# Optimization experiments

Measured on AMD Instinct MI355X. Metric: run time of the kernel, lower is better.

Reference implementation:

```python
import jax, jax.numpy as jnp
import numpy as np

EPS = 1e-6

def elu1(x):
    return jax.nn.elu(x) + 1.0

def causal_linear_attention(q, k, v, chunk=128):
    # q,k,v: [b,h,s,d]; standard (elu+1) linear attention with causal cumulative
    # normalization, computed chunk-wise with a lax.scan carrying the kv state.
    b, h, s, d = q.shape
    sq, sk = elu1(q), elu1(k)
    nc = s // chunk
    rs = lambda x: x.reshape(b, h, nc, chunk, d).transpose(2, 0, 1, 3, 4)  # [nc,b,h,L,d]
    sqc, skc, vc = rs(sq), rs(sk), rs(v)
    mask = jnp.tril(jnp.ones((chunk, chunk), dtype=q.dtype))

    def step(carry, xs):
        S, z = carry  # S: [b,h,d,d] running sum of k^T v; z: [b,h,d] running sum of k
        qc, kc, vcc = xs
        scores = jnp.einsum('bhid,bhjd->bhij', qc, kc) * mask
        num = jnp.einsum('bhij,bhje->bhie', scores, vcc) + jnp.einsum('bhid,bhde->bhie', qc, S)
        den = scores.sum(-1) + jnp.einsum('bhid,bhd->bhi', qc, z)
        out = num / jnp.clip(den, EPS)[..., None]
        S = S + jnp.einsum('bhjd,bhje->bhde', kc, vcc)
        z = z + kc.sum(2)
        return (S, z), out

    S0 = jnp.zeros((b, h, d, d), q.dtype)
    z0 = jnp.zeros((b, h, d), q.dtype)
    _, outs = jax.lax.scan(step, (S0, z0), (sqc, skc, vc))
    return outs.transpose(1, 2, 0, 3, 4).reshape(b, h, s, d)

def setup_inputs() -> dict:
    B, S, H, NH, NM = 2, 4096, 2048, 16, 4
    HD = H // NH
    key = jax.random.key(0)
    ks = jax.random.split(key, 12)
    p = lambda k, shp: (jax.random.normal(k, shp, dtype=jnp.float32) * 0.02)
    return {
        'hidden_states': jax.random.normal(ks[0], (B, S, H), dtype=jnp.float32),
        'w_q': p(ks[1], (H, H)),
        'w_k': p(ks[2], (H, H)),
        'w_v': p(ks[3], (H, H)),
        'w_o': p(ks[4], (H, H)),
        'eg_w1': p(ks[5], (H // 4, H)),
        'eg_b1': jnp.zeros((H // 4,), jnp.float32),
        'eg_w2': p(ks[6], (1, H // 4)),
        'eg_b2': jnp.zeros((1,), jnp.float32),
        'memory_gate': jnp.zeros((NH,), jnp.float32),
        'fine_memories': jax.random.uniform(ks[7], (NM, NH, HD, HD), dtype=jnp.float32) * 0.1,
        'fine_memory_norms': jax.random.uniform(ks[8], (NM, NH, HD), dtype=jnp.float32) + 0.1,
    }

def reference(hidden_states, w_q, w_k, w_v, w_o, eg_w1, eg_b1, eg_w2, eg_b2,
              memory_gate, fine_memories, fine_memory_norms):
    B, S, H = hidden_states.shape
    NH = memory_gate.shape[0]
    HD = H // NH
    split = lambda x: x.reshape(B, S, NH, HD).transpose(0, 2, 1, 3)  # [b,h,s,d]
    q = split(hidden_states @ w_q.T)
    k = split(hidden_states @ w_k.T)
    v = split(hidden_states @ w_v.T)
    sq = elu1(q)

    # coarse memory = sum of fine banks
    M = fine_memories.sum(0)            # [h,d,d]
    z = fine_memory_norms.sum(0)        # [h,d]
    a_c = jnp.einsum('bhsd,hde->bhse', sq, M)
    n_c = jnp.clip(jnp.einsum('bhsd,hd->bhs', sq, z), EPS)[..., None]
    out_coarse = jnp.where(z.sum() < EPS, 0.0, a_c / n_c)

    # fine-grained retrieval over banks, softmax-weighted by relevance
    a_f = jnp.einsum('bhsd,mhde->mbhse', sq, fine_memories)
    n_f = jnp.einsum('bhsd,mhd->mbhs', sq, fine_memory_norms)
    bank_dead = (fine_memory_norms.sum((1, 2)) < EPS)[:, None, None, None, None]
    outs = jnp.where(bank_dead, 0.0, a_f / jnp.clip(n_f, EPS)[..., None])
    rel = n_f.mean(-1)  # [m,b,h]
    w = jax.nn.softmax(rel, axis=0)[..., None, None]  # [m,b,h,1,1]
    out_fine = (outs * w).sum(0)

    # learned expansion gate from coarse representation
    coarse_repr = out_coarse.transpose(0, 2, 1, 3).reshape(B, S, H)
    gprob = jax.nn.sigmoid(jax.nn.relu(coarse_repr @ eg_w1.T + eg_b1) @ eg_w2.T + eg_b2)  # [b,s,1]
    exp_prob = gprob.transpose(0, 2, 1)[..., None]  # [b,1,s,1]

    memory_output = exp_prob * out_fine + (1.0 - exp_prob) * out_coarse
    local_output = causal_linear_attention(q, k, v)
    gate = jax.nn.sigmoid(memory_gate).reshape(1, NH, 1, 1)
    output = gate * memory_output + (1.0 - gate) * local_output
    output = output.transpose(0, 2, 1, 3).reshape(B, S, H)
    return output @ w_o.T
```

## Files before the change

kernel.cpp:

```cpp
#include <hip/hip_runtime.h>

typedef unsigned short ush;
typedef short s16x8 __attribute__((ext_vector_type(8)));
typedef float f32x4 __attribute__((ext_vector_type(4)));

#define Bv 2
#define Sv 4096
#define Hv 2048
#define NHv 16
#define HDv 128
#define NMv 4
#define Tv (Bv*Sv)
#define CHv 128
#define NCv (Sv/CHv)
#define EPSf 1e-6f
#define NTHc ((size_t)Tv*Hv)

__device__ __forceinline__ float b2f(ush u){ return __uint_as_float(((unsigned)u)<<16); }
__device__ __forceinline__ ush f2b(float f){
  unsigned x = __float_as_uint(f);
  return (ush)((x + 0x7fffu + ((x>>16)&1u)) >> 16);
}
__device__ __forceinline__ float lo16(unsigned u){ return b2f((ush)(u & 0xffffu)); }
__device__ __forceinline__ float hi16(unsigned u){ return b2f((ush)(u >> 16)); }
__device__ __forceinline__ unsigned pack2(float a, float b){ return (unsigned)f2b(a) | ((unsigned)f2b(b) << 16); }
__device__ __forceinline__ float elu1f(float x){ return x > 0.f ? x + 1.f : __expf(x); }
__device__ __forceinline__ float sigm(float x){ return 1.f/(1.f + __expf(-x)); }

__device__ __forceinline__ void gload_lds16(const ush* g, ush* l) {
  __builtin_amdgcn_global_load_lds((const __attribute__((address_space(1))) unsigned int*)g,
                                   (__attribute__((address_space(3))) unsigned int*)l, 16, 0, 0);
}

__global__ void probe_kernel(float* out, float val){ out[0] = val; }

__global__ __launch_bounds__(256)
void cvt_kernel(const float* __restrict__ in, ush* __restrict__ out, int n8)
{
  int i = blockIdx.x * 256 + threadIdx.x;
  if (i >= n8) return;
  const float4* p = (const float4*)in + (size_t)i*2;
  float4 x = p[0], y = p[1];
  ushort4 a; a.x=f2b(x.x); a.y=f2b(x.y); a.z=f2b(x.z); a.w=f2b(x.w);
  ushort4 b; b.x=f2b(y.x); b.y=f2b(y.y); b.z=f2b(y.z); b.w=f2b(y.w);
  *(ushort4*)(out + (size_t)i*8)     = a;
  *(ushort4*)(out + (size_t)i*8 + 4) = b;
}

__global__ __launch_bounds__(256)
void fmt_kernel(const float* __restrict__ fm, ush* __restrict__ fmt)
{
  int mh = blockIdx.x;
  const float* src = fm + (size_t)mh*HDv*HDv;
  ush* dst = fmt + (size_t)mh*HDv*HDv;
  __shared__ ush T[HDv][HDv+4];
  #pragma unroll 4
  for (int l = 0; l < 64; ++l) {
    int idx = threadIdx.x + l*256;
    int d = idx >> 7, e = idx & 127;
    T[d][e] = f2b(src[idx]);
  }
  __syncthreads();
  #pragma unroll 4
  for (int l = 0; l < 64; ++l) {
    int idx = threadIdx.x + l*256;
    int e = idx >> 7, d = idx & 127;
    dst[idx] = T[d][e];
  }
}

__global__ __launch_bounds__(256)
void tp_kernel(const ush* __restrict__ src, ush* __restrict__ dst)
{
  int blk = blockIdx.x;
  int st = blk & 31, bh = blk >> 5;
  int h = bh & 15, b = bh >> 4;
  size_t t0 = (size_t)b*Sv + st*128;
  int hcol = h*HDv;
  __shared__ __align__(16) ush T[128*128];
  int tid = threadIdx.x;
  #pragma unroll
  for (int l = 0; l < 8; ++l) {
    int idx = tid + l*256;
    int row = idx >> 4, c8 = (idx & 15) << 3;
    *(uint4*)(T + row*128 + c8) = *(const uint4*)(src + (t0 + row)*Hv + hcol + c8);
  }
  __syncthreads();
  #pragma unroll
  for (int l = 0; l < 8; ++l) {
    int idx = tid + l*256;
    int d = idx & 127, t8 = (idx >> 7) << 3;
    ush tmp[8];
    #pragma unroll
    for (int q = 0; q < 8; ++q) tmp[q] = T[(t8 + q)*128 + d];
    *(uint4*)(dst + ((size_t)bh*HDv + d)*Sv + st*128 + t8) = *(uint4*)tmp;
  }
}

template<int OBF, int EPQ>
__global__ __launch_bounds__(512)
void gemm8(const ush* __restrict__ A, const ush* __restrict__ B,
           ush* __restrict__ C0, ush* __restrict__ C1, ush* __restrict__ C2,
           float* __restrict__ Cf, int N, int K)
{
  __shared__ __align__(16) ush LDS[3*16384 + 3*8192];
  ush* Atb = LDS;
  ush* Btb = LDS + 3*16384;
  const int tid = threadIdx.x, lane = tid & 63, w = tid >> 6;
  const int wr = w >> 1, wn = w & 1;
  const int la = lane & 15, lk = lane >> 4;

  int nwg = gridDim.x;
  int bid = blockIdx.x;
  int lin = (bid & 7) * (nwg >> 3) + (bid >> 3);
  int NBX = N >> 7;
  int by = lin / NBX, bx = lin % NBX;
  int bm = by << 8, bn = bx << 7;

  auto stage = [&](int t){
    int kt = t << 6;
    ush* Ad = Atb + (t % 3) * 16384;
    ush* Bd = Btb + (t % 3) * 8192;
    #pragma unroll
    for (int c = 0; c < 4; ++c) {
      int idx = tid + c*512;
      int row = idx >> 3, sl = idx & 7;
      gload_lds16(A + (size_t)(bm + row)*K + kt + ((sl ^ (row & 7))*8),
                  Ad + (w*64 + c*512)*8);
    }
    #pragma unroll
    for (int c = 0; c < 2; ++c) {
      int idx = tid + c*512;
      int row = idx >> 3, sl = idx & 7;
      gload_lds16(B + (size_t)(bn + row)*K + kt + ((sl ^ (row & 7))*8),
                  Bd + (w*64 + c*512)*8);
    }
  };

  f32x4 acc[4][4];
  #pragma unroll
  for (int i = 0; i < 4; ++i)
    #pragma unroll
    for (int j = 0; j < 4; ++j) acc[i][j] = (f32x4){0.f,0.f,0.f,0.f};

  stage(0);
  stage(1);
  const int nt = 32;
  for (int t = 0; t < nt; ++t) {
    if (t < nt-2) {
      stage(t + 2);
      asm volatile("s_waitcnt vmcnt(12)" ::: "memory");
    } else if (t == nt-2) {
      asm volatile("s_waitcnt vmcnt(6)" ::: "memory");
    } else {
      asm volatile("s_waitcnt vmcnt(0)" ::: "memory");
    }
    __builtin_amdgcn_s_barrier();
    __builtin_amdgcn_sched_barrier(0);

    const ush* Ab = Atb + (t % 3) * 16384;
    const ush* Bb = Btb + (t % 3) * 8192;
    __builtin_amdgcn_s_setprio(1);
    #pragma unroll
    for (int kk = 0; kk < 2; ++kk) {
      s16x8 a[4], b[4];
      int ks = kk*4 + lk;
      #pragma unroll
      for (int f = 0; f < 4; ++f) {
        int ar = wr*64 + f*16 + la;
        a[f] = *(const s16x8*)(Ab + ar*64 + ((ks ^ (ar & 7))*8));
        int br = wn*64 + f*16 + la;
        b[f] = *(const s16x8*)(Bb + br*64 + ((ks ^ (br & 7))*8));
      }
      #pragma unroll
      for (int i = 0; i < 4; ++i)
        #pragma unroll
        for (int j = 0; j < 4; ++j)
          acc[i][j] = __builtin_amdgcn_mfma_f32_16x16x32_bf16(a[i], b[j], acc[i][j], 0, 0, 0);
    }
    __builtin_amdgcn_s_setprio(0);
    __builtin_amdgcn_sched_barrier(0);
    __builtin_amdgcn_s_barrier();
  }

  int seg = bn >> 11;
  if (OBF) {
    ush* Cb = LDS;
    #pragma unroll
    for (int i = 0; i < 4; ++i)
      #pragma unroll
      for (int j = 0; j < 4; ++j)
        #pragma unroll
        for (int r = 0; r < 4; ++r) {
          int row = wr*64 + i*16 + lk*4 + r;
          int col = wn*64 + j*16 + la;
          float v = acc[i][j][r];
          if (EPQ && seg < 2) v = elu1f(v);
          Cb[row*136 + col] = f2b(v);
        }
    __syncthreads();
    ush* outp = (seg == 0) ? C0 : (seg == 1) ? C1 : C2;
    int col0 = bn & 2047;
    #pragma unroll
    for (int l = 0; l < 8; ++l) {
      int chunk = tid + l*512;
      int row = chunk >> 4, cc = chunk & 15;
      *(uint4*)(outp + (size_t)(bm + row)*2048 + col0 + cc*8) = *(const uint4*)(Cb + row*136 + cc*8);
    }
  } else {
    float* Cb = (float*)LDS;
    #pragma unroll
    for (int i = 0; i < 4; ++i)
      #pragma unroll
      for (int j = 0; j < 4; ++j)
        #pragma unroll
        for (int r = 0; r < 4; ++r) {
          int row = wr*64 + i*16 + lk*4 + r;
          int col = wn*64 + j*16 + la;
          Cb[row*132 + col] = acc[i][j][r];
        }
    __syncthreads();
    #pragma unroll
    for (int l = 0; l < 16; ++l) {
      int chunk = tid + l*512;
      int row = chunk >> 5, cc = chunk & 31;
      *(float4*)(Cf + (size_t)(bm + row)*N + bn + cc*4) = *(const float4*)(Cb + row*132 + cc*4);
    }
  }
}

template<int OBF, int EP>
__global__ __launch_bounds__(256)
void gemm_bf(const ush* __restrict__ A, const ush* __restrict__ B,
             const float* __restrict__ bias, void* __restrict__ Cv,
             int M, int N, int K)
{
  __shared__ __align__(16) ush As[128*64];
  __shared__ __align__(16) ush Bs[128*64];
  const int tid = threadIdx.x;
  const int lane = tid & 63;
  const int w = tid >> 6;
  const int wr = w >> 1, wc = w & 1;
  const int bm = blockIdx.y * 128, bn = blockIdx.x * 128;

  f32x4 acc[4][4];
  #pragma unroll
  for (int i = 0; i < 4; ++i)
    #pragma unroll
    for (int j = 0; j < 4; ++j) acc[i][j] = (f32x4){0.f,0.f,0.f,0.f};

  const int srow = lane >> 3;
  const int sslot = lane & 7;
  const int la = lane & 15;
  const int lk = lane >> 4;

  for (int kt = 0; kt < K; kt += 64) {
    #pragma unroll
    for (int r = 0; r < 4; ++r) {
      int row = r*32 + w*8 + srow;
      int kg = sslot ^ (row & 7);
      gload_lds16(A + (size_t)(bm + row)*K + kt + kg*8, (ush*)((char*)As + (r*32 + w*8)*128));
      gload_lds16(B + (size_t)(bn + row)*K + kt + kg*8, (ush*)((char*)Bs + (r*32 + w*8)*128));
    }
    __syncthreads();
    #pragma unroll
    for (int ks = 0; ks < 2; ++ks) {
      s16x8 a[4], b[4];
      int kslot = ks*4 + lk;
      #pragma unroll
      for (int f = 0; f < 4; ++f) {
        int arow = wr*64 + f*16 + la;
        a[f] = *(const s16x8*)((const char*)As + arow*128 + ((kslot ^ (arow & 7))*16));
        int brow = wc*64 + f*16 + la;
        b[f] = *(const s16x8*)((const char*)Bs + brow*128 + ((kslot ^ (brow & 7))*16));
      }
      #pragma unroll
      for (int i = 0; i < 4; ++i)
        #pragma unroll
        for (int j = 0; j < 4; ++j)
          acc[i][j] = __builtin_amdgcn_mfma_f32_16x16x32_bf16(a[i], b[j], acc[i][j], 0, 0, 0);
    }
    __syncthreads();
  }
  #pragma unroll
  for (int i = 0; i < 4; ++i) {
    int rbase = bm + wr*64 + i*16 + lk*4;
    #pragma unroll
    for (int j = 0; j < 4; ++j) {
      int col = bn + wc*64 + j*16 + la;
      #pragma unroll
      for (int r = 0; r < 4; ++r) {
        float vv = acc[i][j][r];
        if (EP == 1) vv = elu1f(vv);
        else if (EP == 2) vv = fmaxf(vv + bias[col], 0.f);
        int row = rbase + r;
        if (OBF) ((ush*)Cv)[(size_t)row*N + col] = f2b(vv);
        else     ((float*)Cv)[(size_t)row*N + col] = vv;
      }
    }
  }
}

__global__ void prep_kernel(const float* __restrict__ norms, const float* __restrict__ mg,
                            float* __restrict__ zsum, float* __restrict__ gate)
{
  int idx = blockIdx.x * 256 + threadIdx.x;
  if (idx < NHv*HDv) {
    float s = 0.f;
    #pragma unroll
    for (int m = 0; m < NMv; ++m) s += norms[m*NHv*HDv + idx];
    zsum[idx] = s;
  }
  if (idx < NHv) gate[idx] = sigm(mg[idx]);
}

__global__ void prep2_kernel(const float* __restrict__ norms, float* __restrict__ bdead,
                             float* __restrict__ ztot, float* __restrict__ rel)
{
  int tid = threadIdx.x;
  float pm[NMv] = {0.f,0.f,0.f,0.f};
  for (int i = tid; i < NHv*HDv; i += 256)
    #pragma unroll
    for (int m = 0; m < NMv; ++m) pm[m] += norms[m*NHv*HDv + i];
  __shared__ float red[4][NMv];
  #pragma unroll
  for (int m = 0; m < NMv; ++m) {
    float v = pm[m];
    for (int off = 32; off; off >>= 1) v += __shfl_down(v, off, 64);
    if ((tid & 63) == 0) red[tid >> 6][m] = v;
  }
  __syncthreads();
  if (tid == 0) {
    float tot = 0.f;
    #pragma unroll
    for (int m = 0; m < NMv; ++m) {
      float s = red[0][m] + red[1][m] + red[2][m] + red[3][m];
      bdead[m] = (s < EPSf) ? 1.f : 0.f;
      tot += s;
    }
    ztot[0] = tot;
  }
  if (tid < NMv*Bv*NHv) rel[tid] = 0.f;
}

__global__ __launch_bounds__(256)
void nf_kernel(const ush* __restrict__ sq, const float* __restrict__ norms,
               const float* __restrict__ zsum, float* __restrict__ nf5,
               float* __restrict__ rel)
{
  int blk = blockIdx.x;
  int st = blk % (Sv/256);
  int bh = blk / (Sv/256);
  int h = bh & 15, b = bh >> 4;
  int tid = threadIdx.x;
  __shared__ float nrm[5][HDv];
  for (int i = tid; i < 5*HDv; i += 256) {
    int m = i / HDv, d = i % HDv;
    nrm[m][d] = (m < NMv) ? norms[(m*NHv + h)*HDv + d] : zsum[h*HDv + d];
  }
  __syncthreads();
  int s = st*256 + tid;
  size_t t = (size_t)b*Sv + s;
  const ush* qp = sq + t*Hv + h*HDv;
  float acc[5] = {0.f,0.f,0.f,0.f,0.f};
  #pragma unroll 4
  for (int d0 = 0; d0 < HDv; d0 += 8) {
    uint4 u = *(const uint4*)(qp + d0);
    float q[8];
    q[0]=lo16(u.x); q[1]=hi16(u.x); q[2]=lo16(u.y); q[3]=hi16(u.y);
    q[4]=lo16(u.z); q[5]=hi16(u.z); q[6]=lo16(u.w); q[7]=hi16(u.w);
    #pragma unroll
    for (int e = 0; e < 8; ++e)
      #pragma unroll
      for (int m = 0; m < 5; ++m) acc[m] = fmaf(q[e], nrm[m][d0+e], acc[m]);
  }
  #pragma unroll
  for (int m = 0; m < 5; ++m) nf5[((size_t)m*Bv*NHv + bh)*Sv + s] = acc[m];
  __shared__ float redl[4][NMv];
  #pragma unroll
  for (int m = 0; m < NMv; ++m) {
    float v = acc[m];
    for (int off = 32; off; off >>= 1) v += __shfl_down(v, off, 64);
    if ((tid & 63) == 0) redl[tid >> 6][m] = v;
  }
  __syncthreads();
  if (tid < NMv) {
    float sm = redl[0][tid] + redl[1][tid] + redl[2][tid] + redl[3][tid];
    atomicAdd(&rel[tid*Bv*NHv + bh], sm);
  }
}

__global__ void softmax_rel(const float* __restrict__ rel, float* __restrict__ wsm)
{
  int i = threadIdx.x;
  if (i >= Bv*NHv) return;
  float r[NMv], mx = -1e30f;
  #pragma unroll
  for (int m = 0; m < NMv; ++m) { r[m] = rel[m*Bv*NHv + i] / (float)Sv; mx = fmaxf(mx, r[m]); }
  float se = 0.f;
  #pragma unroll
  for (int m = 0; m < NMv; ++m) { r[m] = __expf(r[m] - mx); se += r[m]; }
  #pragma unroll
  for (int m = 0; m < NMv; ++m) wsm[m*Bv*NHv + i] = r[m] / se;
}

__global__ __launch_bounds__(512)
void finecoarse_mfma(const ush* __restrict__ sq, const ush* __restrict__ fmt,
                     const float* __restrict__ nf5, const float* __restrict__ wsm,
                     const float* __restrict__ bdead, const float* __restrict__ ztot,
                     ush* __restrict__ fineO, ush* __restrict__ coarseO)
{
  __shared__ __align__(16) ush Qs[2*128*64];
  __shared__ __align__(16) ush Fs[2*128*64];
  __shared__ float scl[NMv][128];
  __shared__ float csc[128];

  int blk = blockIdx.x;
  int tt = blk & 31; int bh = blk >> 5;
  int h = bh & 15, b = bh >> 4;
  size_t t0 = (size_t)b*Sv + tt*128;
  int hcol = h*HDv;
  int tid = threadIdx.x;
  int lane = tid & 63, w = tid >> 6;
  int wr = w >> 2, wc = w & 3;
  int srow = lane >> 3, sslot = lane & 7;
  int la = lane & 15, lk = lane >> 4;

  #pragma unroll
  for (int kh = 0; kh < 2; ++kh)
    #pragma unroll
    for (int r = 0; r < 2; ++r) {
      int row = r*64 + w*8 + srow;
      int kg = sslot ^ (row & 7);
      gload_lds16(sq + (t0 + row)*Hv + hcol + kh*64 + kg*8,
                  Qs + kh*8192 + (r*64 + w*8)*64);
    }
  if (tid < 128) {
    int s = tt*128 + tid;
    float nc = nf5[((size_t)4*Bv*NHv + bh)*Sv + s];
    csc[tid] = (ztot[0] >= EPSf) ? 1.f/fmaxf(nc, EPSf) : 0.f;
    #pragma unroll
    for (int m = 0; m < NMv; ++m) {
      float nfm = nf5[((size_t)m*Bv*NHv + bh)*Sv + s];
      scl[m][tid] = (bdead[m] > 0.5f) ? 0.f : wsm[m*Bv*NHv + bh]/fmaxf(nfm, EPSf);
    }
  }

  f32x4 accF[4][2], accC[4][2];
  #pragma unroll
  for (int i = 0; i < 4; ++i)
    #pragma unroll
    for (int j = 0; j < 2; ++j) { accF[i][j] = (f32x4){0,0,0,0}; accC[i][j] = (f32x4){0,0,0,0}; }

  for (int m = 0; m < NMv; ++m) {
    const ush* F = fmt + (size_t)(m*NHv + h)*HDv*HDv;
    #pragma unroll
    for (int kh = 0; kh < 2; ++kh)
      #pragma unroll
      for (int r = 0; r < 2; ++r) {
        int row = r*64 + w*8 + srow;
        int kg = sslot ^ (row & 7);
        gload_lds16(F + (size_t)row*HDv + kh*64 + kg*8,
                    Fs + kh*8192 + (r*64 + w*8)*64);
      }
    __syncthreads();
    f32x4 P[4][2];
    #pragma unroll
    for (int i = 0; i < 4; ++i)
      #pragma unroll
      for (int j = 0; j < 2; ++j) P[i][j] = (f32x4){0,0,0,0};
    #pragma unroll
    for (int kh = 0; kh < 2; ++kh)
      #pragma unroll
      for (int ks = 0; ks < 2; ++ks) {
        s16x8 a[4], bq[2];
        int kslot = ks*4 + lk;
        #pragma unroll
        for (int f = 0; f < 4; ++f) {
          int arow = wr*64 + f*16 + la;
          a[f] = *(const s16x8*)(Qs + kh*8192 + arow*64 + ((kslot ^ (arow & 7))*8));
        }
        #pragma unroll
        for (int f = 0; f < 2; ++f) {
          int brow = wc*32 + f*16 + la;
          bq[f] = *(const s16x8*)(Fs + kh*8192 + brow*64 + ((kslot ^ (brow & 7))*8));
        }
        #pragma unroll
        for (int i = 0; i < 4; ++i)
          #pragma unroll
          for (int j = 0; j < 2; ++j)
            P[i][j] = __builtin_amdgcn_mfma_f32_16x16x32_bf16(a[i], bq[j], P[i][j], 0, 0, 0);
      }
    #pragma unroll
    for (int i = 0; i < 4; ++i) {
      float sm[4];
      #pragma unroll
      for (int r = 0; r < 4; ++r) sm[r] = scl[m][wr*64 + i*16 + lk*4 + r];
      #pragma unroll
      for (int j = 0; j < 2; ++j)
        #pragma unroll
        for (int r = 0; r < 4; ++r) {
          accF[i][j][r] = fmaf(sm[r], P[i][j][r], accF[i][j][r]);
          accC[i][j][r] += P[i][j][r];
        }
    }
    __syncthreads();
  }
  #pragma unroll
  for (int i = 0; i < 4; ++i)
    #pragma unroll
    for (int r = 0; r < 4; ++r) {
      int row = wr*64 + i*16 + lk*4 + r;
      float cs = csc[row];
      size_t gro = (t0 + row)*Hv + hcol;
      #pragma unroll
      for (int j = 0; j < 2; ++j) {
        int col = wc*32 + j*16 + la;
        fineO[gro + col]   = f2b(accF[i][j][r]);
        coarseO[gro + col] = f2b(accC[i][j][r]*cs);
      }
    }
}

__global__ __launch_bounds__(64)
void gprob_kernel(const float* __restrict__ g1, const float* __restrict__ w2,
                  const float* __restrict__ b2, float* __restrict__ gprob)
{
  int t = blockIdx.x, l = threadIdx.x;
  float s = 0.f;
  #pragma unroll
  for (int i = l; i < Hv/4; i += 64) s = fmaf(g1[(size_t)t*(Hv/4) + i], w2[i], s);
  for (int off = 32; off; off >>= 1) s += __shfl_down(s, off, 64);
  if (l == 0) gprob[t] = sigm(s + b2[0]);
}

__global__ __launch_bounds__(512)
void kv_chunk_mfma(const ush* __restrict__ kT, const ush* __restrict__ vT,
                   float* __restrict__ KVc, float* __restrict__ zc)
{
  __shared__ __align__(16) ush Vt[128*128];
  __shared__ __align__(16) ush Kt[128*128];
  int blk = blockIdx.x;
  int c = blk & 31, bh = blk >> 5;
  const ush* kg = kT + (size_t)bh*HDv*Sv + c*CHv;
  const ush* vg = vT + (size_t)bh*HDv*Sv + c*CHv;
  int tid = threadIdx.x, lane = tid & 63, w = tid >> 6;
  int wr = w >> 2, wc = w & 3;
  int la = lane & 15, lk = lane >> 4;
  int srow4 = lane >> 4, sslot = lane & 15;

  #pragma unroll
  for (int r = 0; r < 4; ++r) {
    int row = r*32 + w*4 + srow4;
    int slot = sslot ^ (row & 7);
    gload_lds16(vg + (size_t)row*Sv + slot*8, Vt + (r*32 + w*4)*128);
    gload_lds16(kg + (size_t)row*Sv + slot*8, Kt + (r*32 + w*4)*128);
  }
  __syncthreads();

  if (tid < 128) {
    float zacc = 0.f;
    int rx = tid & 7;
    #pragma unroll
    for (int s = 0; s < 16; ++s) {
      const ush* p = Kt + tid*128 + ((s ^ rx)*8);
      #pragma unroll
      for (int q = 0; q < 8; ++q) zacc += b2f(p[q]);
    }
    zc[(size_t)blk*HDv + tid] = zacc;
  }

  f32x4 acc[4][2];
  #pragma unroll
  for (int i = 0; i < 4; ++i)
    #pragma unroll
    for (int j = 0; j < 2; ++j) acc[i][j] = (f32x4){0,0,0,0};
  #pragma unroll
  for (int kw = 0; kw < 4; ++kw) {
    s16x8 a[4], b[2];
    int slot = kw*4 + lk;
    #pragma unroll
    for (int f = 0; f < 4; ++f) {
      int ar = wr*64 + f*16 + la;
      a[f] = *(const s16x8*)(Vt + ar*128 + ((slot ^ (ar & 7))*8));
    }
    #pragma unroll
    for (int f = 0; f < 2; ++f) {
      int br = wc*32 + f*16 + la;
      b[f] = *(const s16x8*)(Kt + br*128 + ((slot ^ (br & 7))*8));
    }
    #pragma unroll
    for (int i = 0; i < 4; ++i)
      #pragma unroll
      for (int j = 0; j < 2; ++j)
        acc[i][j] = __builtin_amdgcn_mfma_f32_16x16x32_bf16(a[i], b[j], acc[i][j], 0, 0, 0);
  }
  size_t obase = (size_t)blk*(HDv*HDv);
  #pragma unroll
  for (int i = 0; i < 4; ++i)
    #pragma unroll
    for (int j = 0; j < 2; ++j)
      #pragma unroll
      for (int r = 0; r < 4; ++r) {
        int e = wr*64 + i*16 + lk*4 + r;
        int d = wc*32 + j*16 + la;
        KVc[obase + e*HDv + d] = acc[i][j][r];
      }
}

__global__ __launch_bounds__(256)
void scan_kernel(const float* __restrict__ KVc, ush* __restrict__ kvt, float* __restrict__ zc)
{
  int blk = blockIdx.x;
  int dg = blk & 7; int bh = blk >> 3;
  int tid = threadIdx.x;
  float Sreg[8];
  #pragma unroll
  for (int k = 0; k < 8; ++k) Sreg[k] = 0.f;
  float zreg = 0.f;
  for (int c = 0; c < NCv; ++c) {
    size_t base = ((size_t)bh*NCv + c)*(HDv*HDv) + dg*2048;
    #pragma unroll
    for (int k = 0; k < 8; ++k) {
      size_t idx = base + tid + k*256;
      float tmp = KVc[idx];
      kvt[idx] = f2b(Sreg[k]);
      Sreg[k] += tmp;
    }
    if (dg == 0 && tid < HDv) {
      size_t zb = ((size_t)bh*NCv + c)*HDv + tid;
      float tmp = zc[zb];
      zc[zb] = zreg;
      zreg += tmp;
    }
  }
}

__global__ __launch_bounds__(512)
void attn_chunk_mfma(const ush* __restrict__ sq, const ush* __restrict__ sk,
                     const ush* __restrict__ vT, const ush* __restrict__ kvt,
                     const float* __restrict__ zc, ush* __restrict__ outl)
{
  __shared__ __align__(16) ush Qs[128*128];
  __shared__ __align__(16) ush Ks[128*128];
  __shared__ __align__(16) ush Vs[128*128];
  __shared__ __align__(16) ush Ss[128*128];
  __shared__ float densP[4][128];
  __shared__ float dens[128];

  int blk = blockIdx.x;
  int c = blk & 31, bh = blk >> 5;
  int h = bh & 15, b = bh >> 4;
  size_t t0 = (size_t)b*Sv + c*CHv;
  int hcol = h*HDv;
  int tid = threadIdx.x, lane = tid & 63, w = tid >> 6;
  int wr = w >> 2, wc = w & 3;
  int la = lane & 15, lk = lane >> 4;
  int srow4 = lane >> 4, sslot = lane & 15;
  const float* zcg = zc + (size_t)blk*HDv;

  const ush* qg = sq + t0*Hv + hcol;
  const ush* kg = sk + t0*Hv + hcol;
  const ush* vg = vT + (size_t)bh*HDv*Sv + c*CHv;
  const ush* sg = kvt + (size_t)blk*(HDv*HDv);
  #pragma unroll
  for (int r = 0; r < 4; ++r) {
    int row = r*32 + w*4 + srow4;
    int slot = sslot ^ (row & 7);
    int lb = (r*32 + w*4)*128;
    gload_lds16(qg + (size_t)row*Hv + slot*8, Qs + lb);
    gload_lds16(kg + (size_t)row*Hv + slot*8, Ks + lb);
    gload_lds16(vg + (size_t)row*Sv + slot*8, Vs + lb);
    gload_lds16(sg + row*HDv + slot*8, Ss + lb);
  }
  __syncthreads();

  f32x4 sc[4][2];
  #pragma unroll
  for (int i = 0; i < 4; ++i)
    #pragma unroll
    for (int j = 0; j < 2; ++j) sc[i][j] = (f32x4){0,0,0,0};
  #pragma unroll
  for (int kw = 0; kw < 4; ++kw) {
    s16x8 a[4], b[2];
    int slot = kw*4 + lk;
    #pragma unroll
    for (int f = 0; f < 4; ++f) {
      int ar = wr*64 + f*16 + la;
      a[f] = *(const s16x8*)(Qs + ar*128 + ((slot ^ (ar & 7))*8));
    }
    #pragma unroll
    for (int f = 0; f < 2; ++f) {
      int br = wc*32 + f*16 + la;
      b[f] = *(const s16x8*)(Ks + br*128 + ((slot ^ (br & 7))*8));
    }
    #pragma unroll
    for (int i = 0; i < 4; ++i)
      #pragma unroll
      for (int j = 0; j < 2; ++j)
        sc[i][j] = __builtin_amdgcn_mfma_f32_16x16x32_bf16(a[i], b[j], sc[i][j], 0, 0, 0);
  }
  __syncthreads();
  #pragma unroll
  for (int i = 0; i < 4; ++i)
    #pragma unroll
    for (int j = 0; j < 2; ++j)
      #pragma unroll
      for (int r = 0; r < 4; ++r) {
        int ii = wr*64 + i*16 + lk*4 + r;
        int jj = wc*32 + j*16 + la;
        float v = (jj <= ii) ? sc[i][j][r] : 0.f;
        Ks[ii*128 + (((jj >> 3) ^ (ii & 7))*8) + (jj & 7)] = f2b(v);
      }
  __syncthreads();

  {
    int row = tid & 127, qt = tid >> 7;
    int rx = row & 7;
    float s = 0.f;
    #pragma unroll
    for (int s8 = 0; s8 < 4; ++s8) {
      int slot = qt*4 + s8;
      const ush* p  = Ks + row*128 + ((slot ^ rx)*8);
      const ush* pq = Qs + row*128 + ((slot ^ rx)*8);
      #pragma unroll
      for (int q = 0; q < 8; ++q) s += b2f(p[q]);
      #pragma unroll
      for (int q = 0; q < 8; ++q) s = fmaf(b2f(pq[q]), zcg[slot*8 + q], s);
    }
    densP[qt][row] = s;
  }
  __syncthreads();
  if (tid < 128)
    dens[tid] = fmaxf(densP[0][tid] + densP[1][tid] + densP[2][tid] + densP[3][tid], EPSf);
  __syncthreads();

  f32x4 acc[4][2];
  #pragma unroll
  for (int i = 0; i < 4; ++i)
    #pragma unroll
    for (int j = 0; j < 2; ++j) acc[i][j] = (f32x4){0,0,0,0};
  #pragma unroll
  for (int kw = 0; kw < 4; ++kw) {
    s16x8 a[4], b[2];
    int slot = kw*4 + lk;
    #pragma unroll
    for (int f = 0; f < 4; ++f) {
      int ar = wr*64 + f*16 + la;
      a[f] = *(const s16x8*)(Ks + ar*128 + ((slot ^ (ar & 7))*8));
    }
    #pragma unroll
    for (int f = 0; f < 2; ++f) {
      int br = wc*32 + f*16 + la;
      b[f] = *(const s16x8*)(Vs + br*128 + ((slot ^ (br & 7))*8));
    }
    #pragma unroll
    for (int i = 0; i < 4; ++i)
      #pragma unroll
      for (int j = 0; j < 2; ++j)
        acc[i][j] = __builtin_amdgcn_mfma_f32_16x16x32_bf16(a[i], b[j], acc[i][j], 0, 0, 0);
  }
  #pragma unroll
  for (int kw = 0; kw < 4; ++kw) {
    s16x8 a[4], b[2];
    int slot = kw*4 + lk;
    #pragma unroll
    for (int f = 0; f < 4; ++f) {
      int ar = wr*64 + f*16 + la;
      a[f] = *(const s16x8*)(Qs + ar*128 + ((slot ^ (ar & 7))*8));
    }
    #pragma unroll
    for (int f = 0; f < 2; ++f) {
      int br = wc*32 + f*16 + la;
      b[f] = *(const s16x8*)(Ss + br*128 + ((slot ^ (br & 7))*8));
    }
    #pragma unroll
    for (int i = 0; i < 4; ++i)
      #pragma unroll
      for (int j = 0; j < 2; ++j)
        acc[i][j] = __builtin_amdgcn_mfma_f32_16x16x32_bf16(a[i], b[j], acc[i][j], 0, 0, 0);
  }
  #pragma unroll
  for (int i = 0; i < 4; ++i)
    #pragma unroll
    for (int r = 0; r < 4; ++r) {
      int ii = wr*64 + i*16 + lk*4 + r;
      float inv = 1.f / dens[ii];
      ush* orow = outl + (t0 + ii)*Hv + hcol;
      #pragma unroll
      for (int j = 0; j < 2; ++j) {
        int ee = wc*32 + j*16 + la;
        orow[ee] = f2b(acc[i][j][r]*inv);
      }
    }
}

__global__ __launch_bounds__(256)
void combine_kernel(const ush* __restrict__ fine, const ush* __restrict__ coarse,
                    const ush* __restrict__ local, const float* __restrict__ gprob,
                    const float* __restrict__ gate, ush* __restrict__ comb)
{
  size_t idx = (size_t)blockIdx.x * 256 + threadIdx.x;
  if (idx >= NTHc/8) return;
  size_t fi = idx * 8;
  int t = (int)(fi / Hv);
  int h = (int)((fi % Hv) >> 7);
  float g = gate[h];
  float p = gprob[t];
  uint4 uf = *(const uint4*)(fine + fi);
  uint4 uc = *(const uint4*)(coarse + fi);
  uint4 ul = *(const uint4*)(local + fi);
  uint4 o;
  unsigned* ufp = (unsigned*)&uf; unsigned* ucp = (unsigned*)&uc;
  unsigned* ulp = (unsigned*)&ul; unsigned* op = (unsigned*)&o;
  #pragma unroll
  for (int wq = 0; wq < 4; ++wq) {
    float f0 = lo16(ufp[wq]), f1 = hi16(ufp[wq]);
    float c0 = lo16(ucp[wq]), c1 = hi16(ucp[wq]);
    float l0 = lo16(ulp[wq]), l1 = hi16(ulp[wq]);
    float o0 = g*(p*f0 + (1.f-p)*c0) + (1.f-g)*l0;
    float o1 = g*(p*f1 + (1.f-p)*c1) + (1.f-g)*l1;
    op[wq] = pack2(o0, o1);
  }
  *(uint4*)(comb + fi) = o;
}

extern "C" void kernel_launch(void* const* d_in, const int* in_sizes, int n_in,
                              void* d_out, int out_size, void* d_ws, size_t ws_size,
                              hipStream_t stream)
{
  (void)in_sizes; (void)n_in; (void)out_size;
  const float* hs    = (const float*)d_in[0];
  const float* w_q   = (const float*)d_in[1];
  const float* w_k   = (const float*)d_in[2];
  const float* w_v   = (const float*)d_in[3];
  const float* w_o   = (const float*)d_in[4];
  const float* eg_w1 = (const float*)d_in[5];
  const float* eg_b1 = (const float*)d_in[6];
  const float* eg_w2 = (const float*)d_in[7];
  const float* eg_b2 = (const float*)d_in[8];
  const float* mg    = (const float*)d_in[9];
  const float* fm    = (const float*)d_in[10];
  const float* norms = (const float*)d_in[11];

  probe_kernel<<<1, 1, 0, stream>>>((float*)d_out, (float)(ws_size >> 20));

  char* W = (char*)d_ws;
  size_t o = 0;
  auto take = [&](size_t bytes) -> char* {
    char* p = W + o;
    o += (bytes + 255) & ~(size_t)255;
    return p;
  };
  ush* hs_bf = (ush*)take(NTHc * 2);
  ush* kT = hs_bf;
  ush* local_bf = hs_bf;
  char* R2 = take(NTHc * 4);
  ush* wq_bf = (ush*)R2;
  ush* wk_bf = (ush*)(R2 + (size_t)Hv*Hv*2);
  ush* wv_bf = (ush*)(R2 + (size_t)Hv*Hv*4);
  float* kvc = (float*)R2;
  ush* fine_bf = (ush*)R2;
  float* g1 = (float*)(R2 + NTHc*2);
  ush* wo_bf   = (ush*)take((size_t)Hv*Hv*2);
  ush* egw1_bf = (ush*)take((size_t)(Hv/4)*Hv*2);
  ush* sq_bf = (ush*)take(NTHc * 2);  ush* comb = sq_bf;
  ush* sk_bf = (ush*)take(NTHc * 2);
  ush* v_bf  = (ush*)take(NTHc * 2);
  ush* kvt_bf = v_bf;
  ush* vT = (ush*)take(NTHc * 2);
  ush* coarse_bf = vT;
  float* zcb  = (float*)take((size_t)Bv*NHv*NCv*HDv * 4);
  float* nf5  = (float*)take((size_t)5*Bv*NHv*Sv * 4);
  ush* fmt_bf = (ush*)take((size_t)NMv*NHv*HDv*HDv * 2);
  float* rel  = (float*)take(NMv*Bv*NHv * 4);
  float* wsm  = (float*)take(NMv*Bv*NHv * 4);
  float* gprob= (float*)take((size_t)Tv * 4);
  float* zsum = (float*)take(NHv*HDv * 4);
  float* gate = (float*)take(NHv * 4);
  float* bdead= (float*)take(NMv * 4);
  float* ztot = (float*)take(4);
  if (ws_size < o) return;

  cvt_kernel<<<(int)(NTHc/8/256), 256, 0, stream>>>(hs, hs_bf, (int)(NTHc/8));
  cvt_kernel<<<(int)((size_t)Hv*Hv/8/256), 256, 0, stream>>>(w_q, wq_bf, Hv*Hv/8);
  cvt_kernel<<<(int)((size_t)Hv*Hv/8/256), 256, 0, stream>>>(w_k, wk_bf, Hv*Hv/8);
  cvt_kernel<<<(int)((size_t)Hv*Hv/8/256), 256, 0, stream>>>(w_v, wv_bf, Hv*Hv/8);
  cvt_kernel<<<(int)((size_t)Hv*Hv/8/256), 256, 0, stream>>>(w_o, wo_bf, Hv*Hv/8);
  cvt_kernel<<<(int)((size_t)(Hv/4)*Hv/8/256), 256, 0, stream>>>(eg_w1, egw1_bf, (Hv/4)*Hv/8);
  fmt_kernel<<<NMv*NHv, 256, 0, stream>>>(fm, fmt_bf);

  prep_kernel<<<(NHv*HDv + 255)/256, 256, 0, stream>>>(norms, mg, zsum, gate);
  prep2_kernel<<<1, 256, 0, stream>>>(norms, bdead, ztot, rel);

  gemm8<1,1><<<(6144/128)*(Tv/256), 512, 0, stream>>>(hs_bf, wq_bf, sq_bf, sk_bf, v_bf,
                                                      nullptr, 6144, Hv);

  tp_kernel<<<Bv*NHv*32, 256, 0, stream>>>(sk_bf, kT);
  tp_kernel<<<Bv*NHv*32, 256, 0, stream>>>(v_bf, vT);

  nf_kernel<<<Bv*NHv*(Sv/256), 256, 0, stream>>>(sq_bf, norms, zsum, nf5, rel);
  softmax_rel<<<1, 64, 0, stream>>>(rel, wsm);

  kv_chunk_mfma<<<Bv*NHv*NCv, 512, 0, stream>>>(kT, vT, kvc, zcb);
  scan_kernel<<<Bv*NHv*8, 256, 0, stream>>>(kvc, kvt_bf, zcb);
  attn_chunk_mfma<<<Bv*NHv*NCv, 512, 0, stream>>>(sq_bf, sk_bf, vT, kvt_bf, zcb, local_bf);

  finecoarse_mfma<<<Bv*NHv*32, 512, 0, stream>>>(sq_bf, fmt_bf, nf5, wsm, bdead, ztot, fine_bf, coarse_bf);

  gemm_bf<0,2><<<dim3((Hv/4)/128, Tv/128), 256, 0, stream>>>(coarse_bf, egw1_bf, eg_b1, g1, Tv, Hv/4, Hv);
  gprob_kernel<<<Tv, 64, 0, stream>>>(g1, eg_w2, eg_b2, gprob);

  combine_kernel<<<(int)(NTHc/8/256), 256, 0, stream>>>(fine_bf, coarse_bf, local_bf, gprob, gate, comb);

  gemm8<0,0><<<(2048/128)*(Tv/256), 512, 0, stream>>>(comb, wo_bf, nullptr, nullptr, nullptr,
                                                      (float*)d_out, 2048, Hv);
}
```

Before: 623.3 us.

## Route gate GEMM through pipelined gemm8 and remap tile order into column panels

```diff
diff --git a/kernel.cpp b/kernel.cpp
--- a/kernel.cpp
+++ b/kernel.cpp
@@ -100,6 +100,7 @@
 template<int OBF, int EPQ>
 __global__ __launch_bounds__(512)
 void gemm8(const ush* __restrict__ A, const ush* __restrict__ B,
+           const float* __restrict__ bias,
            ush* __restrict__ C0, ush* __restrict__ C1, ush* __restrict__ C2,
            float* __restrict__ Cf, int N, int K)
 {
@@ -110,11 +111,18 @@
   const int wr = w >> 1, wn = w & 1;
   const int la = lane & 15, lk = lane >> 4;
 
-  int nwg = gridDim.x;
   int bid = blockIdx.x;
-  int lin = (bid & 7) * (nwg >> 3) + (bid >> 3);
   int NBX = N >> 7;
-  int by = lin / NBX, bx = lin % NBX;
+  int by, bx;
+  if (NBX >= 8) {
+    int panel = bid >> 8;
+    int rem = bid & 255;
+    bx = panel*8 + (rem & 7);
+    by = rem >> 3;
+  } else {
+    bx = bid % NBX;
+    by = bid / NBX;
+  }
   int bm = by << 8, bn = bx << 7;
 
   auto stage = [&](int t){
@@ -195,7 +203,7 @@
           int row = wr*64 + i*16 + lk*4 + r;
           int col = wn*64 + j*16 + la;
           float v = acc[i][j][r];
-          if (EPQ && seg < 2) v = elu1f(v);
+          if (EPQ == 1 && seg < 2) v = elu1f(v);
           Cb[row*136 + col] = f2b(v);
         }
     __syncthreads();
@@ -217,7 +225,9 @@
         for (int r = 0; r < 4; ++r) {
           int row = wr*64 + i*16 + lk*4 + r;
           int col = wn*64 + j*16 + la;
-          Cb[row*132 + col] = acc[i][j][r];
+          float v = acc[i][j][r];
+          if (EPQ == 2) v = fmaxf(v + bias[bn + col], 0.f);
+          Cb[row*132 + col] = v;
         }
     __syncthreads();
     #pragma unroll
@@ -225,78 +235,6 @@
       int chunk = tid + l*512;
       int row = chunk >> 5, cc = chunk & 31;
       *(float4*)(Cf + (size_t)(bm + row)*N + bn + cc*4) = *(const float4*)(Cb + row*132 + cc*4);
-    }
-  }
-}
-
-template<int OBF, int EP>
-__global__ __launch_bounds__(256)
-void gemm_bf(const ush* __restrict__ A, const ush* __restrict__ B,
-             const float* __restrict__ bias, void* __restrict__ Cv,
-             int M, int N, int K)
-{
-  __shared__ __align__(16) ush As[128*64];
-  __shared__ __align__(16) ush Bs[128*64];
-  const int tid = threadIdx.x;
-  const int lane = tid & 63;
-  const int w = tid >> 6;
-  const int wr = w >> 1, wc = w & 1;
-  const int bm = blockIdx.y * 128, bn = blockIdx.x * 128;
-
-  f32x4 acc[4][4];
-  #pragma unroll
-  for (int i = 0; i < 4; ++i)
-    #pragma unroll
-    for (int j = 0; j < 4; ++j) acc[i][j] = (f32x4){0.f,0.f,0.f,0.f};
-
-  const int srow = lane >> 3;
-  const int sslot = lane & 7;
-  const int la = lane & 15;
-  const int lk = lane >> 4;
-
-  for (int kt = 0; kt < K; kt += 64) {
-    #pragma unroll
-    for (int r = 0; r < 4; ++r) {
-      int row = r*32 + w*8 + srow;
-      int kg = sslot ^ (row & 7);
-      gload_lds16(A + (size_t)(bm + row)*K + kt + kg*8, (ush*)((char*)As + (r*32 + w*8)*128));
-      gload_lds16(B + (size_t)(bn + row)*K + kt + kg*8, (ush*)((char*)Bs + (r*32 + w*8)*128));
-    }
-    __syncthreads();
-    #pragma unroll
-    for (int ks = 0; ks < 2; ++ks) {
-      s16x8 a[4], b[4];
-      int kslot = ks*4 + lk;
-      #pragma unroll
-      for (int f = 0; f < 4; ++f) {
-        int arow = wr*64 + f*16 + la;
-        a[f] = *(const s16x8*)((const char*)As + arow*128 + ((kslot ^ (arow & 7))*16));
-        int brow = wc*64 + f*16 + la;
-        b[f] = *(const s16x8*)((const char*)Bs + brow*128 + ((kslot ^ (brow & 7))*16));
-      }
-      #pragma unroll
-      for (int i = 0; i < 4; ++i)
-        #pragma unroll
-        for (int j = 0; j < 4; ++j)
-          acc[i][j] = __builtin_amdgcn_mfma_f32_16x16x32_bf16(a[i], b[j], acc[i][j], 0, 0, 0);
-    }
-    __syncthreads();
-  }
-  #pragma unroll
-  for (int i = 0; i < 4; ++i) {
-    int rbase = bm + wr*64 + i*16 + lk*4;
-    #pragma unroll
-    for (int j = 0; j < 4; ++j) {
-      int col = bn + wc*64 + j*16 + la;
-      #pragma unroll
-      for (int r = 0; r < 4; ++r) {
-        float vv = acc[i][j][r];
-        if (EP == 1) vv = elu1f(vv);
-        else if (EP == 2) vv = fmaxf(vv + bias[col], 0.f);
-        int row = rbase + r;
-        if (OBF) ((ush*)Cv)[(size_t)row*N + col] = f2b(vv);
-        else     ((float*)Cv)[(size_t)row*N + col] = vv;
-      }
     }
   }
 }
@@ -893,8 +831,8 @@
   prep_kernel<<<(NHv*HDv + 255)/256, 256, 0, stream>>>(norms, mg, zsum, gate);
   prep2_kernel<<<1, 256, 0, stream>>>(norms, bdead, ztot, rel);
 
-  gemm8<1,1><<<(6144/128)*(Tv/256), 512, 0, stream>>>(hs_bf, wq_bf, sq_bf, sk_bf, v_bf,
-                                                      nullptr, 6144, Hv);
+  gemm8<1,1><<<(6144/128)*(Tv/256), 512, 0, stream>>>(hs_bf, wq_bf, nullptr,
+                                                      sq_bf, sk_bf, v_bf, nullptr, 6144, Hv);
 
   tp_kernel<<<Bv*NHv*32, 256, 0, stream>>>(sk_bf, kT);
   tp_kernel<<<Bv*NHv*32, 256, 0, stream>>>(v_bf, vT);
@@ -908,11 +846,12 @@
 
   finecoarse_mfma<<<Bv*NHv*32, 512, 0, stream>>>(sq_bf, fmt_bf, nf5, wsm, bdead, ztot, fine_bf, coarse_bf);
 
-  gemm_bf<0,2><<<dim3((Hv/4)/128, Tv/128), 256, 0, stream>>>(coarse_bf, egw1_bf, eg_b1, g1, Tv, Hv/4, Hv);
+  gemm8<0,2><<<(512/128)*(Tv/256), 512, 0, stream>>>(coarse_bf, egw1_bf, eg_b1,
+                                                     nullptr, nullptr, nullptr, g1, 512, Hv);
   gprob_kernel<<<Tv, 64, 0, stream>>>(g1, eg_w2, eg_b2, gprob);
 
   combine_kernel<<<(int)(NTHc/8/256), 256, 0, stream>>>(fine_bf, coarse_bf, local_bf, gprob, gate, comb);
 
-  gemm8<0,0><<<(2048/128)*(Tv/256), 512, 0, stream>>>(comb, wo_bf, nullptr, nullptr, nullptr,
-                                                      (float*)d_out, 2048, Hv);
-}
+  gemm8<0,0><<<(2048/128)*(Tv/256), 512, 0, stream>>>(comb, wo_bf, nullptr,
+                                                      nullptr, nullptr, nullptr, (float*)d_out, 2048, Hv);
+}
```

Measured after the change: 659.5 us. +5.8%, slower.
